# Kernel optimization log

Measured on AMD Instinct MI355X. Metric: run time of the kernel, lower is better.

## Reference

```python
import jax, jax.numpy as jnp
import numpy as np

B, S, D = 4, 2048, 1024
H = 16
DH = D // H


def setup_inputs() -> dict:
    key = jax.random.key(0)
    ks = jax.random.split(key, 5)
    scale = 1.0 / np.sqrt(D)
    return {
        "x": jax.random.normal(ks[0], (B, S, D), dtype=jnp.float32),
        "wq": jax.random.normal(ks[1], (D, D), dtype=jnp.float32) * scale,
        "wk": jax.random.normal(ks[2], (D, D), dtype=jnp.float32) * scale,
        "wv": jax.random.normal(ks[3], (D, D), dtype=jnp.float32) * scale,
        "wo": jax.random.normal(ks[4], (D, D), dtype=jnp.float32) * scale,
    }


def reference(x, wq, wk, wv, wo):
    b, s, d = x.shape
    # nn.Linear applies x @ W.T (weights are [out, in])
    q = (x @ wq.T).reshape(b, s, H, DH).transpose(0, 2, 1, 3)  # [b,h,s,dh]
    k = (x @ wk.T).reshape(b, s, H, DH).transpose(0, 2, 1, 3)
    v = (x @ wv.T).reshape(b, s, H, DH).transpose(0, 2, 1, 3)
    scale = 1.0 / jnp.sqrt(jnp.asarray(DH, dtype=x.dtype))
    scores = jnp.einsum("bhqd,bhkd->bhqk", q, k) * scale  # [b,h,s,s]
    causal = jnp.tril(jnp.ones((s, s), dtype=bool))
    scores = jnp.where(causal, scores, -jnp.inf)
    attn = jax.nn.softmax(scores, axis=-1)
    out = jnp.einsum("bhqk,bhkd->bhqd", attn, v)  # [b,h,s,dh]
    out = out.transpose(0, 2, 1, 3).reshape(b, s, d)
    return out @ wo.T
```

## Files before the change

### kernel.cpp

```cpp
#include <hip/hip_runtime.h>
#include <hip/hip_bf16.h>

#define Bz 4
#define Sz 2048
#define Dz 1024
#define Hz 16
#define DHz 64

typedef __bf16 bf16x8 __attribute__((ext_vector_type(8)));
typedef float f32x4 __attribute__((ext_vector_type(4)));
typedef short s16x4 __attribute__((ext_vector_type(4)));
typedef short s16x8 __attribute__((ext_vector_type(8)));
typedef unsigned short u16x4 __attribute__((ext_vector_type(4)));

#define SCQF 0.18033688011112042f

__global__ __launch_bounds__(256) void cvt_all(const float* __restrict__ x,
                                               const float* __restrict__ w0, const float* __restrict__ w1,
                                               const float* __restrict__ w2, const float* __restrict__ w3,
                                               __hip_bfloat16* __restrict__ dst) {
    constexpr int TOK = Bz * Sz * Dz;
    constexpr int WEL = Dz * Dz;
    int i = (blockIdx.x * 256 + threadIdx.x) * 4;
    const float* src;
    if (i < TOK) {
        src = x + i;
    } else {
        const int jj = i - TOK;
        const int which = jj >> 20;
        const float* w = (which == 0) ? w0 : (which == 1) ? w1 : (which == 2) ? w2 : w3;
        src = w + (jj & (WEL - 1));
    }
    float4 f = *reinterpret_cast<const float4*>(src);
    dst[i + 0] = __float2bfloat16(f.x);
    dst[i + 1] = __float2bfloat16(f.y);
    dst[i + 2] = __float2bfloat16(f.z);
    dst[i + 3] = __float2bfloat16(f.w);
}

__device__ __forceinline__ void gl2lds16(const __hip_bfloat16* g, __hip_bfloat16* l) {
    __builtin_amdgcn_global_load_lds(
        (const __attribute__((address_space(1))) void*)g,
        (__attribute__((address_space(3))) void*)l, 16, 0, 0);
}

__device__ __forceinline__ unsigned ldsaddr(const void* p) {
    return (unsigned)(size_t)(const __attribute__((address_space(3))) void*)p;
}

template <int N, int K, typename OT, int MODE, bool SCQ = false>
__device__ __forceinline__ void gemm128_body(const __hip_bfloat16* __restrict__ A,
                                             const __hip_bfloat16* __restrict__ W,
                                             OT* __restrict__ C, int bm, int bn,
                                             __hip_bfloat16* As, __hip_bfloat16* Bs) {
    const int tid  = threadIdx.x;
    const int wid  = tid >> 6;
    const int lane = tid & 63;
    const int quad = lane >> 4;
    const int l16  = lane & 15;
    const int wr = wid >> 1, wc = wid & 1;

    const int rlo = lane >> 3;
    const int xel = ((lane & 7) ^ rlo) * 8;
    const __hip_bfloat16* gA = A + (size_t)(bm * 128 + wid * 32 + rlo) * K + xel;
    const __hip_bfloat16* gB = W + (size_t)(bn * 128 + wid * 32 + rlo) * K + xel;
    __hip_bfloat16* lA = &As[(wid * 32) * 64];
    __hip_bfloat16* lB = &Bs[(wid * 32) * 64];

    const unsigned sw = (unsigned)((l16 & 7) << 4);
    const char* Ap = (const char*)As;
    const char* Bp = (const char*)Bs;

    f32x4 acc[4][4] = {};

    for (int k0 = 0; k0 < K; k0 += 64) {
        __syncthreads();
#pragma unroll
        for (int c = 0; c < 4; ++c) {
            gl2lds16(gA + (size_t)(c * 8) * K + k0, lA + (c * 8) * 64);
            gl2lds16(gB + (size_t)(c * 8) * K + k0, lB + (c * 8) * 64);
        }
        __syncthreads();

#pragma unroll
        for (int kk = 0; kk < 2; ++kk) {
            bf16x8 af[4], bf[4];
#pragma unroll
            for (int mi = 0; mi < 4; ++mi)
                af[mi] = *reinterpret_cast<const bf16x8*>(
                    Ap + (wr * 64 + mi * 16 + l16) * 128 + ((kk * 64 + quad * 16) ^ sw));
#pragma unroll
            for (int ni = 0; ni < 4; ++ni)
                bf[ni] = *reinterpret_cast<const bf16x8*>(
                    Bp + (wc * 64 + ni * 16 + l16) * 128 + ((kk * 64 + quad * 16) ^ sw));
#pragma unroll
            for (int mi = 0; mi < 4; ++mi)
#pragma unroll
                for (int ni = 0; ni < 4; ++ni)
                    acc[mi][ni] = __builtin_amdgcn_mfma_f32_16x16x32_bf16(af[mi], bf[ni], acc[mi][ni], 0, 0, 0);
        }
    }

#pragma unroll
    for (int mi = 0; mi < 4; ++mi)
#pragma unroll
        for (int ni = 0; ni < 4; ++ni) {
            const int row0 = bm * 128 + wr * 64 + mi * 16 + quad * 4;
            const int col  = bn * 128 + wc * 64 + ni * 16 + l16;
#pragma unroll
            for (int r = 0; r < 4; ++r) {
                const int row = row0 + r;
                float v = acc[mi][ni][r];
                if constexpr (SCQ) v *= SCQF;
                if constexpr (MODE == 0) {
                    if constexpr (__is_same(OT, float))
                        C[(size_t)row * N + col] = v;
                    else
                        C[(size_t)row * N + col] = __float2bfloat16(v);
                } else if constexpr (MODE == 1) {
                    const int bh = (row >> 11) * Hz + (col >> 6);
                    C[(size_t)bh * (Sz * DHz) + (size_t)(row & 2047) * 64 + (col & 63)] =
                        __float2bfloat16(v);
                } else {
                    const int bh = (row >> 11) * Hz + (col >> 6);
                    C[(size_t)bh * (Sz * DHz) + (size_t)((col >> 4) & 3) * (Sz * 16) +
                      (size_t)(row & 2047) * 16 + (col & 15)] = __float2bfloat16(v);
                }
            }
        }
}

template <int M, int N, int K, typename OT>
__global__ __launch_bounds__(256) void gemm128(const __hip_bfloat16* __restrict__ A,
                                               const __hip_bfloat16* __restrict__ W,
                                               OT* __restrict__ C) {
    __shared__ __hip_bfloat16 As[128 * 64];
    __shared__ __hip_bfloat16 Bs[128 * 64];
    constexpr int NB = N / 128;
    constexpr int NWG = (M / 128) * NB;
    const int bid = blockIdx.x;
    const int swz = (bid & 7) * (NWG / 8) + (bid >> 3);
    gemm128_body<N, K, OT, 0>(A, W, C, swz / NB, swz % NB, As, Bs);
}

template <int M, int K>
__global__ __launch_bounds__(256) void gemm_qkv(const __hip_bfloat16* __restrict__ A,
                                                const __hip_bfloat16* __restrict__ W0,
                                                const __hip_bfloat16* __restrict__ W1,
                                                const __hip_bfloat16* __restrict__ W2,
                                                __hip_bfloat16* __restrict__ C0,
                                                __hip_bfloat16* __restrict__ C1,
                                                __hip_bfloat16* __restrict__ C2) {
    __shared__ __hip_bfloat16 As[128 * 64];
    __shared__ __hip_bfloat16 Bs[128 * 64];
    constexpr int NB = Dz / 128;
    constexpr int NWG = 3 * (M / 128) * NB;
    const int bid = blockIdx.x;
    const int s   = (bid & 7) * (NWG / 8) + (bid >> 3);
    const int which = s % 3;
    const int rem   = s / 3;
    const int bm = rem / NB, bn = rem % NB;
    if (which == 0)      gemm128_body<Dz, K, __hip_bfloat16, 0, true>(A, W0, C0, bm, bn, As, Bs);
    else if (which == 1) gemm128_body<Dz, K, __hip_bfloat16, 1>(A, W1, C1, bm, bn, As, Bs);
    else                 gemm128_body<Dz, K, __hip_bfloat16, 2>(A, W2, C2, bm, bn, As, Bs);
}

__device__ __forceinline__ bf16x8 cat8(s16x4 a, s16x4 b) {
    s16x8 t = __builtin_shufflevector(a, b, 0, 1, 2, 3, 4, 5, 6, 7);
    union { s16x8 s; bf16x8 h; } u; u.s = t; return u.h;
}

#define TRD(i, off) \
    asm volatile("ds_read_b64_tr_b16 %0, %1 offset:" off : "=v"(vf[i]) : "v"(va))

__global__ __launch_bounds__(256, 4) void attn_mfma9(const __hip_bfloat16* __restrict__ Q,
                                                     const __hip_bfloat16* __restrict__ Kh,
                                                     const __hip_bfloat16* __restrict__ Vh,
                                                     __hip_bfloat16* __restrict__ O) {
    __shared__ __hip_bfloat16 Ks[2][64 * 64];
    __shared__ __hip_bfloat16 Vs[2][64 * 64];

    const int tid  = threadIdx.x;
    const int wid  = tid >> 6;
    const int lane = tid & 63;
    const int quad = lane >> 4;
    const int l16  = lane & 15;

    const int xcd  = blockIdx.x & 7;
    const int j    = blockIdx.x >> 3;
    const int bh   = xcd * 8 + (j >> 4);
    const int pair = j & 15;
    const int h    = bh & 15;
    const int b    = bh >> 4;
    const size_t baseQ = (size_t)b * Sz * Dz + (size_t)h * DHz;
    const size_t kvb   = (size_t)bh * (Sz * DHz);

    const int rlo = lane >> 3;
    const int xel = ((lane & 7) ^ rlo) * 8;

    auto stage = [&](int kn, int bf_) {
#pragma unroll
        for (int c = 0; c < 2; ++c) {
            gl2lds16(Kh + kvb + (size_t)(kn + wid * 16 + c * 8 + rlo) * 64 + xel,
                     &Ks[bf_][(wid * 16 + c * 8) * 64]);
            gl2lds16(Vh + kvb + (size_t)wid * (Sz * 16) + (size_t)(kn + c * 32 + (lane >> 1)) * 16 + (lane & 1) * 8,
                     &Vs[bf_][wid * 1024 + c * 512]);
        }
    };

    const unsigned vb0 = ldsaddr(&Vs[0][0]) + lane * 8;
    const unsigned sw  = (l16 & 7) << 4;

    union { s16x8 s; bf16x8 h; } onesu;
#pragma unroll
    for (int i = 0; i < 8; ++i) onesu.s[i] = (short)0x3F80;
    const bf16x8 ones8 = onesu.h;

    int buf = 0;
    stage(0, 0);
    __syncthreads();

#pragma unroll 1
    for (int p = 0; p < 2; ++p) {
        const int qblk  = (p == 0) ? pair : 31 - pair;
        const int q0    = qblk * 64 + wid * 16;
        const int niter = qblk + 1;

        const __hip_bfloat16* qp = Q + baseQ + (size_t)(q0 + l16) * Dz + quad * 8;
        const bf16x8 qf0 = *reinterpret_cast<const bf16x8*>(qp);
        const bf16x8 qf1 = *reinterpret_cast<const bf16x8*>(qp + 32);

        float m = -1e30f;
        f32x4 ot[4] = {};
        f32x4 lacc  = {};

#pragma unroll 1
        for (int it = 0; it < niter; ++it) {
            const int k0 = it * 64;

            f32x4 st[4] = {};
            {
                const char* Kp = (const char*)&Ks[buf][0];
#pragma unroll
                for (int s = 0; s < 4; ++s) {
                    const int rb = (s * 16 + l16) * 128;
                    const bf16x8 a0 = *reinterpret_cast<const bf16x8*>(Kp + rb + ((quad * 16) ^ sw));
                    const bf16x8 a1 = *reinterpret_cast<const bf16x8*>(Kp + rb + ((quad * 16 + 64) ^ sw));
                    st[s] = __builtin_amdgcn_mfma_f32_16x16x32_bf16(a0, qf0, st[s], 0, 0, 0);
                    st[s] = __builtin_amdgcn_mfma_f32_16x16x32_bf16(a1, qf1, st[s], 0, 0, 0);
                }
            }

            const bool more = (it + 1 < niter);
            if (more)        stage(k0 + 64, buf ^ 1);
            else if (p == 0) stage(0,       buf ^ 1);

            float sv[16];
            if (it == niter - 1) {
                const int qrow = q0 + l16;
#pragma unroll
                for (int s = 0; s < 4; ++s)
#pragma unroll
                    for (int r = 0; r < 4; ++r) {
                        const int key = k0 + s * 16 + quad * 4 + r;
                        sv[s * 4 + r] = (key <= qrow) ? st[s][r] : -1e30f;
                    }
            } else {
#pragma unroll
                for (int s = 0; s < 4; ++s)
#pragma unroll
                    for (int r = 0; r < 4; ++r) sv[s * 4 + r] = st[s][r];
            }

            const float p0 = fmaxf(fmaxf(sv[0],  sv[1]),  sv[2]);
            const float p1 = fmaxf(fmaxf(sv[3],  sv[4]),  sv[5]);
            const float p2 = fmaxf(fmaxf(sv[6],  sv[7]),  sv[8]);
            const float p3 = fmaxf(fmaxf(sv[9],  sv[10]), sv[11]);
            const float p4 = fmaxf(fmaxf(sv[12], sv[13]), sv[14]);
            const float p5 = fmaxf(fmaxf(p0, p1), p2);
            float tmax = fmaxf(fmaxf(fmaxf(p5, p3), p4), sv[15]);
            tmax = fmaxf(tmax, __shfl_xor(tmax, 16, 64));
            tmax = fmaxf(tmax, __shfl_xor(tmax, 32, 64));

            const float mnew = fmaxf(m, tmax);
            const bool  skip = __all(tmax <= m);
            if (!skip) {
                const float alpha = __builtin_amdgcn_exp2f(m - mnew);
                m = mnew;
#pragma unroll
                for (int s = 0; s < 4; ++s) ot[s] *= alpha;
                lacc[0] *= alpha;
            }

            float pv[16];
#pragma unroll
            for (int i = 0; i < 16; ++i) pv[i] = __builtin_amdgcn_exp2f(sv[i] - m);

            s16x4 vf[16];
            const unsigned va = vb0 + (unsigned)(buf << 13);
            TRD(0, "0");    TRD(1, "512");  TRD(2, "1024"); TRD(3, "1536");
            TRD(4, "2048"); TRD(5, "2560"); TRD(6, "3072"); TRD(7, "3584");

            union { s16x8 s; bf16x8 h; } u01, u23;
#pragma unroll
            for (int r = 0; r < 4; ++r) {
                union { __hip_bfloat16 hh; short uu; } c0, c1, c2, c3;
                c0.hh = __float2bfloat16(pv[r]);
                c1.hh = __float2bfloat16(pv[4 + r]);
                c2.hh = __float2bfloat16(pv[8 + r]);
                c3.hh = __float2bfloat16(pv[12 + r]);
                u01.s[r]     = c0.uu;
                u01.s[4 + r] = c1.uu;
                u23.s[r]     = c2.uu;
                u23.s[4 + r] = c3.uu;
            }
            const bf16x8 pw01 = u01.h;
            const bf16x8 pw23 = u23.h;

            lacc = __builtin_amdgcn_mfma_f32_16x16x32_bf16(ones8, pw01, lacc, 0, 0, 0);
            lacc = __builtin_amdgcn_mfma_f32_16x16x32_bf16(ones8, pw23, lacc, 0, 0, 0);

            asm volatile("s_waitcnt lgkmcnt(0)" ::: "memory");
            __builtin_amdgcn_sched_barrier(0);
            TRD(8,  "4096"); TRD(9,  "4608"); TRD(10, "5120"); TRD(11, "5632");
            TRD(12, "6144"); TRD(13, "6656"); TRD(14, "7168"); TRD(15, "7680");

            ot[0] = __builtin_amdgcn_mfma_f32_16x16x32_bf16(cat8(vf[0],  vf[1]),  pw01, ot[0], 0, 0, 0);
            ot[0] = __builtin_amdgcn_mfma_f32_16x16x32_bf16(cat8(vf[2],  vf[3]),  pw23, ot[0], 0, 0, 0);
            ot[1] = __builtin_amdgcn_mfma_f32_16x16x32_bf16(cat8(vf[4],  vf[5]),  pw01, ot[1], 0, 0, 0);
            ot[1] = __builtin_amdgcn_mfma_f32_16x16x32_bf16(cat8(vf[6],  vf[7]),  pw23, ot[1], 0, 0, 0);

            asm volatile("s_waitcnt lgkmcnt(0)" ::: "memory");
            __builtin_amdgcn_sched_barrier(0);
            ot[2] = __builtin_amdgcn_mfma_f32_16x16x32_bf16(cat8(vf[8],  vf[9]),  pw01, ot[2], 0, 0, 0);
            ot[2] = __builtin_amdgcn_mfma_f32_16x16x32_bf16(cat8(vf[10], vf[11]), pw23, ot[2], 0, 0, 0);
            ot[3] = __builtin_amdgcn_mfma_f32_16x16x32_bf16(cat8(vf[12], vf[13]), pw01, ot[3], 0, 0, 0);
            ot[3] = __builtin_amdgcn_mfma_f32_16x16x32_bf16(cat8(vf[14], vf[15]), pw23, ot[3], 0, 0, 0);

            __syncthreads();
            buf ^= 1;
        }

        const float linv = 1.f / lacc[0];
        __hip_bfloat16* op = O + baseQ + (size_t)(q0 + l16) * Dz + quad * 4;
#pragma unroll
        for (int sd = 0; sd < 4; ++sd) {
            u16x4 w;
#pragma unroll
            for (int r = 0; r < 4; ++r) {
                union { __hip_bfloat16 hh; unsigned short uu; } cv;
                cv.hh = __float2bfloat16(ot[sd][r] * linv);
                w[r] = cv.uu;
            }
            *reinterpret_cast<u16x4*>(op + sd * 16) = w;
        }
    }
}

extern "C" void kernel_launch(void* const* d_in, const int* in_sizes, int n_in,
                              void* d_out, int out_size, void* d_ws, size_t ws_size,
                              hipStream_t stream) {
    const float* x  = (const float*)d_in[0];
    const float* wq = (const float*)d_in[1];
    const float* wk = (const float*)d_in[2];
    const float* wv = (const float*)d_in[3];
    const float* wo = (const float*)d_in[4];
    float* out = (float*)d_out;

    constexpr int TOK = Bz * Sz * Dz;
    constexpr int WEL = Dz * Dz;

    __hip_bfloat16* xb  = (__hip_bfloat16*)d_ws;
    __hip_bfloat16* wqb = xb  + TOK;
    __hip_bfloat16* wkb = wqb + WEL;
    __hip_bfloat16* wvb = wkb + WEL;
    __hip_bfloat16* wob = wvb + WEL;
    __hip_bfloat16* Qb  = wob + WEL;
    __hip_bfloat16* Kh  = Qb + TOK;
    __hip_bfloat16* Vh  = (__hip_bfloat16*)d_out;
    __hip_bfloat16* Ob  = xb;

    cvt_all<<<(TOK + 4 * WEL) / 4 / 256, 256, 0, stream>>>(x, wq, wk, wv, wo, xb);

    constexpr int M = Bz * Sz;
    constexpr int GB = (M / 128) * (Dz / 128);

    gemm_qkv<M, Dz><<<3 * GB, 256, 0, stream>>>(xb, wqb, wkb, wvb, Qb, Kh, Vh);

    const int ATTN_BLOCKS = Bz * Hz * 16;
    attn_mfma9<<<ATTN_BLOCKS, 256, 0, stream>>>(Qb, Kh, Vh, Ob);

    gemm128<M, Dz, Dz, float><<<GB, 256, 0, stream>>>(Ob, wob, out);
}
```

Measured before the change: 231.2 us.

## Fuse paired causal query blocks into one KV sweep sharing K/V tiles

The attention kernel previously processed its two query blocks (pair and 31-pair) sequentially, each streaming K/V tiles from global memory. Now both blocks are processed in a single loop over the longer block's KV range, and the short block is computed only while its causal range is active. This roughly halves K/V staging loads and barriers for the short block's range. In exchange it doubles live accumulator registers, which may hurt occupancy under the 4-wave launch bound, and it adds divergent-free but branchy per-iteration work.

Result: no change. 233.9 us (+1.2%).

```diff
diff --git a/kernel.cpp b/kernel.cpp
--- a/kernel.cpp
+++ b/kernel.cpp
@@ -170,13 +170,17 @@
     union { s16x8 s; bf16x8 h; } u; u.s = t; return u.h;
 }
 
+__device__ __forceinline__ f32x4 mfma32bf(bf16x8 a, bf16x8 b, f32x4 c) {
+    return __builtin_amdgcn_mfma_f32_16x16x32_bf16(a, b, c, 0, 0, 0);
+}
+
 #define TRD(i, off) \
     asm volatile("ds_read_b64_tr_b16 %0, %1 offset:" off : "=v"(vf[i]) : "v"(va))
 
-__global__ __launch_bounds__(256, 4) void attn_mfma9(const __hip_bfloat16* __restrict__ Q,
-                                                     const __hip_bfloat16* __restrict__ Kh,
-                                                     const __hip_bfloat16* __restrict__ Vh,
-                                                     __hip_bfloat16* __restrict__ O) {
+__global__ __launch_bounds__(256, 4) void attn_mfma10(const __hip_bfloat16* __restrict__ Q,
+                                                      const __hip_bfloat16* __restrict__ Kh,
+                                                      const __hip_bfloat16* __restrict__ Vh,
+                                                      __hip_bfloat16* __restrict__ O) {
     __shared__ __hip_bfloat16 Ks[2][64 * 64];
     __shared__ __hip_bfloat16 Vs[2][64 * 64];
 
@@ -216,62 +220,70 @@
     for (int i = 0; i < 8; ++i) onesu.s[i] = (short)0x3F80;
     const bf16x8 ones8 = onesu.h;
 
+    const int qbA = pair;
+    const int qbB = 31 - pair;
+    const int q0A = qbA * 64 + wid * 16;
+    const int q0B = qbB * 64 + wid * 16;
+    const int niter = qbB + 1;
+
+    const __hip_bfloat16* qpA = Q + baseQ + (size_t)(q0A + l16) * Dz + quad * 8;
+    const __hip_bfloat16* qpB = Q + baseQ + (size_t)(q0B + l16) * Dz + quad * 8;
+    const bf16x8 qfA0 = *reinterpret_cast<const bf16x8*>(qpA);
+    const bf16x8 qfA1 = *reinterpret_cast<const bf16x8*>(qpA + 32);
+    const bf16x8 qfB0 = *reinterpret_cast<const bf16x8*>(qpB);
+    const bf16x8 qfB1 = *reinterpret_cast<const bf16x8*>(qpB + 32);
+
+    float mA = -1e30f, mB = -1e30f;
+    f32x4 otA[4] = {}, otB[4] = {};
+    f32x4 laccA = {}, laccB = {};
+
     int buf = 0;
     stage(0, 0);
     __syncthreads();
 
 #pragma unroll 1
-    for (int p = 0; p < 2; ++p) {
-        const int qblk  = (p == 0) ? pair : 31 - pair;
-        const int q0    = qblk * 64 + wid * 16;
-        const int niter = qblk + 1;
-
-        const __hip_bfloat16* qp = Q + baseQ + (size_t)(q0 + l16) * Dz + quad * 8;
-        const bf16x8 qf0 = *reinterpret_cast<const bf16x8*>(qp);
-        const bf16x8 qf1 = *reinterpret_cast<const bf16x8*>(qp + 32);
-
-        float m = -1e30f;
-        f32x4 ot[4] = {};
-        f32x4 lacc  = {};
-
-#pragma unroll 1
-        for (int it = 0; it < niter; ++it) {
-            const int k0 = it * 64;
-
-            f32x4 st[4] = {};
-            {
-                const char* Kp = (const char*)&Ks[buf][0];
-#pragma unroll
-                for (int s = 0; s < 4; ++s) {
-                    const int rb = (s * 16 + l16) * 128;
-                    const bf16x8 a0 = *reinterpret_cast<const bf16x8*>(Kp + rb + ((quad * 16) ^ sw));
-                    const bf16x8 a1 = *reinterpret_cast<const bf16x8*>(Kp + rb + ((quad * 16 + 64) ^ sw));
-                    st[s] = __builtin_amdgcn_mfma_f32_16x16x32_bf16(a0, qf0, st[s], 0, 0, 0);
-                    st[s] = __builtin_amdgcn_mfma_f32_16x16x32_bf16(a1, qf1, st[s], 0, 0, 0);
+    for (int t = 0; t < niter; ++t) {
+        const int k0 = t * 64;
+        const bool actA = (t <= qbA);
+
+        f32x4 stB[4] = {};
+        f32x4 stA[4] = {};
+        {
+            const char* Kp = (const char*)&Ks[buf][0];
+#pragma unroll
+            for (int s = 0; s < 4; ++s) {
+                const int rb = (s * 16 + l16) * 128;
+                const bf16x8 a0 = *reinterpret_cast<const bf16x8*>(Kp + rb + ((quad * 16) ^ sw));
+                const bf16x8 a1 = *reinterpret_cast<const bf16x8*>(Kp + rb + ((quad * 16 + 64) ^ sw));
+                stB[s] = mfma32bf(a0, qfB0, stB[s]);
+                stB[s] = mfma32bf(a1, qfB1, stB[s]);
+                if (actA) {
+                    stA[s] = mfma32bf(a0, qfA0, stA[s]);
+                    stA[s] = mfma32bf(a1, qfA1, stA[s]);
                 }
             }
-
-            const bool more = (it + 1 < niter);
-            if (more)        stage(k0 + 64, buf ^ 1);
-            else if (p == 0) stage(0,       buf ^ 1);
-
+        }
+
+        if (t + 1 < niter) stage(k0 + 64, buf ^ 1);
+
+        bf16x8 pwA01 = {}, pwA23 = {};
+        if (actA) {
             float sv[16];
-            if (it == niter - 1) {
-                const int qrow = q0 + l16;
+            if (t == qbA) {
+                const int qrow = q0A + l16;
 #pragma unroll
                 for (int s = 0; s < 4; ++s)
 #pragma unroll
                     for (int r = 0; r < 4; ++r) {
                         const int key = k0 + s * 16 + quad * 4 + r;
-                        sv[s * 4 + r] = (key <= qrow) ? st[s][r] : -1e30f;
+                        sv[s * 4 + r] = (key <= qrow) ? stA[s][r] : -1e30f;
                     }
             } else {
 #pragma unroll
                 for (int s = 0; s < 4; ++s)
 #pragma unroll
-                    for (int r = 0; r < 4; ++r) sv[s * 4 + r] = st[s][r];
-            }
-
+                    for (int r = 0; r < 4; ++r) sv[s * 4 + r] = stA[s][r];
+            }
             const float p0 = fmaxf(fmaxf(sv[0],  sv[1]),  sv[2]);
             const float p1 = fmaxf(fmaxf(sv[3],  sv[4]),  sv[5]);
             const float p2 = fmaxf(fmaxf(sv[6],  sv[7]),  sv[8]);
@@ -281,26 +293,18 @@
             float tmax = fmaxf(fmaxf(fmaxf(p5, p3), p4), sv[15]);
             tmax = fmaxf(tmax, __shfl_xor(tmax, 16, 64));
             tmax = fmaxf(tmax, __shfl_xor(tmax, 32, 64));
-
-            const float mnew = fmaxf(m, tmax);
-            const bool  skip = __all(tmax <= m);
+            const float mnew = fmaxf(mA, tmax);
+            const bool  skip = __all(tmax <= mA);
             if (!skip) {
-                const float alpha = __builtin_amdgcn_exp2f(m - mnew);
-                m = mnew;
-#pragma unroll
-                for (int s = 0; s < 4; ++s) ot[s] *= alpha;
-                lacc[0] *= alpha;
-            }
-
+                const float alpha = __builtin_amdgcn_exp2f(mA - mnew);
+                mA = mnew;
+#pragma unroll
+                for (int s = 0; s < 4; ++s) otA[s] *= alpha;
+                laccA[0] *= alpha;
+            }
             float pv[16];
 #pragma unroll
-            for (int i = 0; i < 16; ++i) pv[i] = __builtin_amdgcn_exp2f(sv[i] - m);
-
-            s16x4 vf[16];
-            const unsigned va = vb0 + (unsigned)(buf << 13);
-            TRD(0, "0");    TRD(1, "512");  TRD(2, "1024"); TRD(3, "1536");
-            TRD(4, "2048"); TRD(5, "2560"); TRD(6, "3072"); TRD(7, "3584");
-
+            for (int i = 0; i < 16; ++i) pv[i] = __builtin_amdgcn_exp2f(sv[i] - mA);
             union { s16x8 s; bf16x8 h; } u01, u23;
 #pragma unroll
             for (int r = 0; r < 4; ++r) {
@@ -309,47 +313,135 @@
                 c1.hh = __float2bfloat16(pv[4 + r]);
                 c2.hh = __float2bfloat16(pv[8 + r]);
                 c3.hh = __float2bfloat16(pv[12 + r]);
-                u01.s[r]     = c0.uu;
-                u01.s[4 + r] = c1.uu;
-                u23.s[r]     = c2.uu;
-                u23.s[4 + r] = c3.uu;
-            }
-            const bf16x8 pw01 = u01.h;
-            const bf16x8 pw23 = u23.h;
-
-            lacc = __builtin_amdgcn_mfma_f32_16x16x32_bf16(ones8, pw01, lacc, 0, 0, 0);
-            lacc = __builtin_amdgcn_mfma_f32_16x16x32_bf16(ones8, pw23, lacc, 0, 0, 0);
-
-            asm volatile("s_waitcnt lgkmcnt(0)" ::: "memory");
-            __builtin_amdgcn_sched_barrier(0);
-            TRD(8,  "4096"); TRD(9,  "4608"); TRD(10, "5120"); TRD(11, "5632");
-            TRD(12, "6144"); TRD(13, "6656"); TRD(14, "7168"); TRD(15, "7680");
-
-            ot[0] = __builtin_amdgcn_mfma_f32_16x16x32_bf16(cat8(vf[0],  vf[1]),  pw01, ot[0], 0, 0, 0);
-            ot[0] = __builtin_amdgcn_mfma_f32_16x16x32_bf16(cat8(vf[2],  vf[3]),  pw23, ot[0], 0, 0, 0);
-            ot[1] = __builtin_amdgcn_mfma_f32_16x16x32_bf16(cat8(vf[4],  vf[5]),  pw01, ot[1], 0, 0, 0);
-            ot[1] = __builtin_amdgcn_mfma_f32_16x16x32_bf16(cat8(vf[6],  vf[7]),  pw23, ot[1], 0, 0, 0);
-
-            asm volatile("s_waitcnt lgkmcnt(0)" ::: "memory");
-            __builtin_amdgcn_sched_barrier(0);
-            ot[2] = __builtin_amdgcn_mfma_f32_16x16x32_bf16(cat8(vf[8],  vf[9]),  pw01, ot[2], 0, 0, 0);
-            ot[2] = __builtin_amdgcn_mfma_f32_16x16x32_bf16(cat8(vf[10], vf[11]), pw23, ot[2], 0, 0, 0);
-            ot[3] = __builtin_amdgcn_mfma_f32_16x16x32_bf16(cat8(vf[12], vf[13]), pw01, ot[3], 0, 0, 0);
-            ot[3] = __builtin_amdgcn_mfma_f32_16x16x32_bf16(cat8(vf[14], vf[15]), pw23, ot[3], 0, 0, 0);
-
-            __syncthreads();
-            buf ^= 1;
-        }
-
-        const float linv = 1.f / lacc[0];
-        __hip_bfloat16* op = O + baseQ + (size_t)(q0 + l16) * Dz + quad * 4;
+                u01.s[r] = c0.uu; u01.s[4 + r] = c1.uu;
+                u23.s[r] = c2.uu; u23.s[4 + r] = c3.uu;
+            }
+            pwA01 = u01.h; pwA23 = u23.h;
+            laccA = mfma32bf(ones8, pwA01, laccA);
+            laccA = mfma32bf(ones8, pwA23, laccA);
+        }
+
+        float svB[16];
+        if (t == qbB) {
+            const int qrow = q0B + l16;
+#pragma unroll
+            for (int s = 0; s < 4; ++s)
+#pragma unroll
+                for (int r = 0; r < 4; ++r) {
+                    const int key = k0 + s * 16 + quad * 4 + r;
+                    svB[s * 4 + r] = (key <= qrow) ? stB[s][r] : -1e30f;
+                }
+        } else {
+#pragma unroll
+            for (int s = 0; s < 4; ++s)
+#pragma unroll
+                for (int r = 0; r < 4; ++r) svB[s * 4 + r] = stB[s][r];
+        }
+        {
+            const float p0 = fmaxf(fmaxf(svB[0],  svB[1]),  svB[2]);
+            const float p1 = fmaxf(fmaxf(svB[3],  svB[4]),  svB[5]);
+            const float p2 = fmaxf(fmaxf(svB[6],  svB[7]),  svB[8]);
+            const float p3 = fmaxf(fmaxf(svB[9],  svB[10]), svB[11]);
+            const float p4 = fmaxf(fmaxf(svB[12], svB[13]), svB[14]);
+            const float p5 = fmaxf(fmaxf(p0, p1), p2);
+            float tmax = fmaxf(fmaxf(fmaxf(p5, p3), p4), svB[15]);
+            tmax = fmaxf(tmax, __shfl_xor(tmax, 16, 64));
+            tmax = fmaxf(tmax, __shfl_xor(tmax, 32, 64));
+            const float mnew = fmaxf(mB, tmax);
+            const bool  skip = __all(tmax <= mB);
+            if (!skip) {
+                const float alpha = __builtin_amdgcn_exp2f(mB - mnew);
+                mB = mnew;
+#pragma unroll
+                for (int s = 0; s < 4; ++s) otB[s] *= alpha;
+                laccB[0] *= alpha;
+            }
+        }
+        float pvB[16];
+#pragma unroll
+        for (int i = 0; i < 16; ++i) pvB[i] = __builtin_amdgcn_exp2f(svB[i] - mB);
+
+        s16x4 vf[16];
+        const unsigned va = vb0 + (unsigned)(buf << 13);
+        TRD(0, "0");    TRD(1, "512");  TRD(2, "1024"); TRD(3, "1536");
+        TRD(4, "2048"); TRD(5, "2560"); TRD(6, "3072"); TRD(7, "3584");
+
+        bf16x8 pwB01, pwB23;
+        {
+            union { s16x8 s; bf16x8 h; } u01, u23;
+#pragma unroll
+            for (int r = 0; r < 4; ++r) {
+                union { __hip_bfloat16 hh; short uu; } c0, c1, c2, c3;
+                c0.hh = __float2bfloat16(pvB[r]);
+                c1.hh = __float2bfloat16(pvB[4 + r]);
+                c2.hh = __float2bfloat16(pvB[8 + r]);
+                c3.hh = __float2bfloat16(pvB[12 + r]);
+                u01.s[r] = c0.uu; u01.s[4 + r] = c1.uu;
+                u23.s[r] = c2.uu; u23.s[4 + r] = c3.uu;
+            }
+            pwB01 = u01.h; pwB23 = u23.h;
+        }
+        laccB = mfma32bf(ones8, pwB01, laccB);
+        laccB = mfma32bf(ones8, pwB23, laccB);
+
+        asm volatile("s_waitcnt lgkmcnt(0)" ::: "memory");
+        __builtin_amdgcn_sched_barrier(0);
+        TRD(8,  "4096"); TRD(9,  "4608"); TRD(10, "5120"); TRD(11, "5632");
+        TRD(12, "6144"); TRD(13, "6656"); TRD(14, "7168"); TRD(15, "7680");
+
+        otB[0] = mfma32bf(cat8(vf[0], vf[1]), pwB01, otB[0]);
+        otB[0] = mfma32bf(cat8(vf[2], vf[3]), pwB23, otB[0]);
+        otB[1] = mfma32bf(cat8(vf[4], vf[5]), pwB01, otB[1]);
+        otB[1] = mfma32bf(cat8(vf[6], vf[7]), pwB23, otB[1]);
+        if (actA) {
+            otA[0] = mfma32bf(cat8(vf[0], vf[1]), pwA01, otA[0]);
+            otA[0] = mfma32bf(cat8(vf[2], vf[3]), pwA23, otA[0]);
+            otA[1] = mfma32bf(cat8(vf[4], vf[5]), pwA01, otA[1]);
+            otA[1] = mfma32bf(cat8(vf[6], vf[7]), pwA23, otA[1]);
+        }
+
+        asm volatile("s_waitcnt lgkmcnt(0)" ::: "memory");
+        __builtin_amdgcn_sched_barrier(0);
+        otB[2] = mfma32bf(cat8(vf[8],  vf[9]),  pwB01, otB[2]);
+        otB[2] = mfma32bf(cat8(vf[10], vf[11]), pwB23, otB[2]);
+        otB[3] = mfma32bf(cat8(vf[12], vf[13]), pwB01, otB[3]);
+        otB[3] = mfma32bf(cat8(vf[14], vf[15]), pwB23, otB[3]);
+        if (actA) {
+            otA[2] = mfma32bf(cat8(vf[8],  vf[9]),  pwA01, otA[2]);
+            otA[2] = mfma32bf(cat8(vf[10], vf[11]), pwA23, otA[2]);
+            otA[3] = mfma32bf(cat8(vf[12], vf[13]), pwA01, otA[3]);
+            otA[3] = mfma32bf(cat8(vf[14], vf[15]), pwA23, otA[3]);
+        }
+
+        __syncthreads();
+        buf ^= 1;
+    }
+
+    {
+        const float linv = 1.f / laccA[0];
+        __hip_bfloat16* op = O + baseQ + (size_t)(q0A + l16) * Dz + quad * 4;
 #pragma unroll
         for (int sd = 0; sd < 4; ++sd) {
             u16x4 w;
 #pragma unroll
             for (int r = 0; r < 4; ++r) {
                 union { __hip_bfloat16 hh; unsigned short uu; } cv;
-                cv.hh = __float2bfloat16(ot[sd][r] * linv);
+                cv.hh = __float2bfloat16(otA[sd][r] * linv);
+                w[r] = cv.uu;
+            }
+            *reinterpret_cast<u16x4*>(op + sd * 16) = w;
+        }
+    }
+    {
+        const float linv = 1.f / laccB[0];
+        __hip_bfloat16* op = O + baseQ + (size_t)(q0B + l16) * Dz + quad * 4;
+#pragma unroll
+        for (int sd = 0; sd < 4; ++sd) {
+            u16x4 w;
+#pragma unroll
+            for (int r = 0; r < 4; ++r) {
+                union { __hip_bfloat16 hh; unsigned short uu; } cv;
+                cv.hh = __float2bfloat16(otB[sd][r] * linv);
                 w[r] = cv.uu;
             }
             *reinterpret_cast<u16x4*>(op + sd * 16) = w;
@@ -388,7 +480,7 @@
     gemm_qkv<M, Dz><<<3 * GB, 256, 0, stream>>>(xb, wqb, wkb, wvb, Qb, Kh, Vh);
 
     const int ATTN_BLOCKS = Bz * Hz * 16;
-    attn_mfma9<<<ATTN_BLOCKS, 256, 0, stream>>>(Qb, Kh, Vh, Ob);
+    attn_mfma10<<<ATTN_BLOCKS, 256, 0, stream>>>(Qb, Kh, Vh, Ob);
 
     gemm128<M, Dz, Dz, float><<<GB, 256, 0, stream>>>(Ob, wob, out);
 }
```
